# Kernel tuning notes

Hardware: AMD Instinct MI355X
Metric: run time of the kernel (lower is better)

The kernel has to match this reference:

```python
import jax, jax.numpy as jnp
import numpy as np
import math

D = 768; H = 12; DH = 64; LAT = 512; B = 2; L = 1024


def _rms(x, w, eps=1e-6):
    return w * x * jax.lax.rsqrt(jnp.mean(x * x, axis=-1, keepdims=True) + eps)


def _rope_tables(seq_len, dh):
    inv = 1.0 / (10000.0 ** (np.arange(0, dh, 2, dtype=np.float32) / dh))
    t = np.arange(seq_len, dtype=np.float32)
    f = np.outer(t, inv)
    emb = np.concatenate([f, f], axis=-1)
    return jnp.asarray(np.cos(emb))[None, :, None, :], jnp.asarray(np.sin(emb))[None, :, None, :]


def _rope(x, cos, sin):
    x1, x2 = jnp.split(x, 2, axis=-1)
    return x * cos + jnp.concatenate([-x2, x1], axis=-1) * sin


def setup_inputs():
    key = jax.random.key(0)
    ks = jax.random.split(key, 8)
    s = 0.02
    return {
        'x': jax.random.normal(ks[0], (B, L, D), jnp.float32),
        'w_ln': jnp.ones((D,), jnp.float32),
        'w_compress': jax.random.normal(ks[1], (D, LAT), jnp.float32) * s,
        'w_qkv': jax.random.normal(ks[2], (LAT, 3 * D), jnp.float32) * s,
        'w_reso': jax.random.normal(ks[3], (LAT, H * 4), jnp.float32) * s,
        'w_qn': jnp.ones((DH,), jnp.float32),
        'w_kn': jnp.ones((DH,), jnp.float32),
        'head_decay': jnp.linspace(-3.0, 1.0, H).astype(jnp.float32),
        'temperature': jnp.ones((1,), jnp.float32) * 0.5,
        'w_out_gate': jax.random.normal(ks[4], (LAT, D), jnp.float32) * s,
        'w_proj': jax.random.normal(ks[5], (D, D), jnp.float32) * s,
        'w_memnorm': jnp.ones((D,), jnp.float32),
    }


def reference(x, w_ln, w_compress, w_qkv, w_reso, w_qn, w_kn, head_decay, temperature, w_out_gate, w_proj, w_memnorm):
    cos, sin = _rope_tables(L, DH)
    xn = _rms(x, w_ln)
    latent = jax.nn.silu(xn @ w_compress)                        # (B,L,LAT)
    q, k, v = jnp.split(latent @ w_qkv, 3, axis=-1)
    q = _rope(_rms(q.reshape(B, L, H, DH), w_qn), cos, sin)
    k = _rope(_rms(k.reshape(B, L, H, DH), w_kn), cos, sin)
    v_f = v.reshape(B, L, H, DH)
    q_f = jax.nn.elu(q) + 1.0
    k_f = jax.nn.elu(k) + 1.0
    params = (latent @ w_reso).reshape(B, L, H, 4)
    sem_amp, sem_phase, ctx_amp, ctx_phase = [params[..., i] for i in range(4)]
    sem_phase = jax.nn.sigmoid(sem_phase) * math.pi
    ctx_phase = jax.nn.sigmoid(ctx_phase) * math.pi
    decay = jnp.clip(0.3 + 0.65 * jax.nn.sigmoid(head_decay), 1e-5, 0.999)   # (H,)
    gate = jnp.clip(jax.nn.sigmoid(jax.nn.sigmoid(sem_amp) * jax.nn.sigmoid(ctx_amp)
                                   * jnp.cos(sem_phase - ctx_phase) * temperature[0]) * 1.2 - 0.1,
                    0.05, 0.95)                                  # (B,L,H)
    one_m = (1.0 - decay)[None, None, :]                          # (1,1,H)
    kv_in = jnp.einsum('blhd,blhe->blhde', k_f, v_f) * gate[..., None, None] * one_m[..., None, None]
    z_in = k_f * one_m[..., None]
    # cumulative log-decay -> df, same as torch cumsum of constant per-step log_decay
    cum_log = jnp.arange(1, L + 1, dtype=jnp.float32)[:, None] * jnp.log(decay)[None, :]
    df = jnp.exp(cum_log)[None, :, :, None]                       # (1,L,H,1)
    kv_states = jnp.cumsum(kv_in / (df[..., None] + 1e-8), axis=1) * df[..., None]
    z_states = jnp.cumsum(z_in / (df + 1e-8), axis=1) * df
    out_num = jnp.einsum('blhd,blhde->blhe', q_f, kv_states)
    den = jnp.clip(jnp.sum(q_f * z_states, axis=-1, keepdims=True), 1e-5, None)
    out = (out_num / den).reshape(B, L, D)
    return (_rms(out, w_memnorm) @ w_proj) * jax.nn.silu(latent @ w_out_gate)
```

## Files before the change

kernel.cpp:

```cpp
#include <hip/hip_runtime.h>
#include <hip/hip_bf16.h>
#include <math.h>

#define D_MODEL 768
#define NHEAD   12
#define LATD    512
#define BATCH   2
#define SEQ     1024
#define NROWS   (BATCH*SEQ)
#define NCHUNK  (SEQ/64)
#define NBH     (BATCH*NHEAD)
#define NFUSE   3200
#define PQ      72

using short8 = __attribute__((ext_vector_type(8))) short;
using f32x4  = __attribute__((ext_vector_type(4))) float;

__device__ __forceinline__ float sigf(float x){ return 1.f/(1.f+expf(-x)); }
__device__ __forceinline__ float decay_of(float hd){
  float d = 0.3f + 0.65f*sigf(hd);
  return fminf(fmaxf(d, 1e-5f), 0.999f);
}
__device__ __forceinline__ unsigned short f2b(float f){
  __hip_bfloat16 h = __float2bfloat16(f);
  return *reinterpret_cast<unsigned short*>(&h);
}
__device__ __forceinline__ float bf2f(unsigned short u){
  unsigned int x = ((unsigned int)u) << 16;
  return __uint_as_float(x);
}
__device__ __forceinline__ void async16(const unsigned short* g, unsigned short* l){
  __builtin_amdgcn_global_load_lds((const __attribute__((address_space(1))) void*)g,
                                   (__attribute__((address_space(3))) void*)l, 16, 0, 0);
}

__device__ __forceinline__ void rms_row(const float* __restrict__ xr,
    const float* __restrict__ w, unsigned short* __restrict__ yr,
    int tid, float* red)
{
  float v0 = xr[tid], v1 = xr[tid+256], v2 = xr[tid+512];
  float s = v0*v0 + v1*v1 + v2*v2;
  #pragma unroll
  for (int off=32; off; off>>=1) s += __shfl_xor(s, off, 64);
  if ((tid & 63) == 0) red[tid>>6] = s;
  __syncthreads();
  s = red[0]+red[1]+red[2]+red[3];
  float sc = rsqrtf(s*(1.f/(float)D_MODEL) + 1e-6f);
  yr[tid]     = f2b(v0*sc*w[tid]);
  yr[tid+256] = f2b(v1*sc*w[tid+256]);
  yr[tid+512] = f2b(v2*sc*w[tid+512]);
}

__global__ __launch_bounds__(256) void k_rmsnorm_bf(const float* __restrict__ x,
    const float* __restrict__ w, unsigned short* __restrict__ y)
{
  __shared__ float red[4];
  int row = blockIdx.x, tid = threadIdx.x;
  rms_row(x + (size_t)row*D_MODEL, w, y + (size_t)row*D_MODEL, tid, red);
}

__global__ __launch_bounds__(256) void k_prep(
    const float* __restrict__ x, const float* __restrict__ w_ln,
    unsigned short* __restrict__ xn,
    const float* __restrict__ wc, const float* __restrict__ wq,
    const float* __restrict__ wr, const float* __restrict__ wg,
    const float* __restrict__ wp,
    unsigned short* __restrict__ wtc, unsigned short* __restrict__ wtq,
    unsigned short* __restrict__ wtg, unsigned short* __restrict__ wtp)
{
  __shared__ unsigned short tile[64][65];
  __shared__ float red[4];
  int blk = blockIdx.x, t = threadIdx.x;
  if (blk >= 640){
    int row = blk - 640;
    rms_row(x + (size_t)row*D_MODEL, w_ln, xn + (size_t)row*D_MODEL, t, red);
    return;
  }
  const float* W; unsigned short* WT; int K, N, bx, by;
  if (blk < 96){ W=wc; WT=wtc; K=768; N=512; bx=blk&7; by=blk>>3; }
  else if (blk < 384){ int i=blk-96;  W=wq; WT=wtq; K=512; N=2304; bx=i%36; by=i/36; }
  else if (blk < 480){ int i=blk-384; W=wg; WT=wtg; K=512; N=768;  bx=i%12; by=i/12; }
  else if (blk < 624){ int i=blk-480; W=wp; WT=wtp; K=768; N=768;  bx=i%12; by=i/12; }
  else {
    int i = blk - 624;
    #pragma unroll
    for (int j=0;j<16;j++){
      int e = i*4096 + t + j*256;
      int n = 2304 + (e >> 9), k = e & 511;
      float v = (n < 2352) ? wr[(size_t)k*48 + (n-2304)] : 0.f;
      wtq[(size_t)n*512 + k] = f2b(v);
    }
    return;
  }
  int k0 = by*64, n0 = bx*64, cr = t >> 6, cc = t & 63;
  #pragma unroll
  for (int i=0;i<16;i++){
    int r = cr + i*4;
    tile[r][cc] = f2b(W[(size_t)(k0+r)*N + n0 + cc]);
  }
  __syncthreads();
  #pragma unroll
  for (int i=0;i<16;i++){
    int nn = cr + i*4;
    WT[(size_t)(n0+nn)*K + k0 + cc] = tile[cc][nn];
  }
}

__global__ __launch_bounds__(256) void k_gemm64(const unsigned short* __restrict__ A,
    const unsigned short* __restrict__ BT, float* __restrict__ Cf,
    unsigned short* __restrict__ Cb, const unsigned short* __restrict__ auxb,
    int M, int N, int K, int act)
{
  __shared__ unsigned short As[64*64];
  __shared__ unsigned short Bs[64*64];
  int tid = threadIdx.x;
  int w = tid >> 6, lane = tid & 63;
  int m16 = lane & 15, quad = lane >> 4;
  int bm = blockIdx.y*64, bn = blockIdx.x*64;

  f32x4 acc[4];
  #pragma unroll
  for (int nt=0;nt<4;nt++) acc[nt] = (f32x4){0.f,0.f,0.f,0.f};

  for (int kk = 0; kk < K; kk += 64){
    #pragma unroll
    for (int i=0;i<2;i++){
      int g = (w*2 + i)*64 + lane;
      int m = g >> 3, c = (g & 7) ^ (m & 7);
      async16(A  + (size_t)(bm+m)*K + kk + c*8, As + (w*2+i)*512);
      async16(BT + (size_t)(bn+m)*K + kk + c*8, Bs + (w*2+i)*512);
    }
    __syncthreads();
    #pragma unroll
    for (int s=0;s<2;s++){
      int row = w*16 + m16;
      short8 af = *(const short8*)(As + (row*8 + ((s*4 + quad) ^ (row & 7)))*8);
      #pragma unroll
      for (int nt=0;nt<4;nt++){
        int n = nt*16 + m16;
        short8 bf = *(const short8*)(Bs + (n*8 + ((s*4 + quad) ^ (n & 7)))*8);
        acc[nt] = __builtin_amdgcn_mfma_f32_16x16x32_bf16(af, bf, acc[nt], 0, 0, 0);
      }
    }
    __syncthreads();
  }
  #pragma unroll
  for (int r=0;r<4;r++){
    int row = bm + w*16 + quad*4 + r;
    #pragma unroll
    for (int nt=0;nt<4;nt++){
      int col = bn + nt*16 + m16;
      float v = acc[nt][r];
      if (act == 1) v = v/(1.f + __expf(-v));
      else if (act == 2) v *= bf2f(auxb[(size_t)row*N + col]);
      if (Cf) Cf[(size_t)row*N + col] = v;
      if (Cb) Cb[(size_t)row*N + col] = f2b(v);
    }
  }
}

__global__ __launch_bounds__(256) void k_gemm_fused(const unsigned short* __restrict__ A,
    const unsigned short* __restrict__ BT, const float* __restrict__ w_qn,
    const float* __restrict__ w_kn, const float* __restrict__ hdec,
    const float* __restrict__ temp, unsigned short* __restrict__ qf,
    unsigned short* __restrict__ kf, unsigned short* __restrict__ vf,
    float* __restrict__ cKV, float* __restrict__ cG,
    unsigned short* __restrict__ gateb)
{
  __shared__ __align__(16) unsigned short SM[2*128*64];
  unsigned short* As = SM;
  unsigned short* Bs = SM + 128*64;
  const int K = LATD;
  int tid = threadIdx.x;
  int w = tid >> 6, lane = tid & 63;
  int wm = (w >> 1)*64, wn = (w & 1)*64;
  int m16 = lane & 15, quad = lane >> 4;
  int bm = blockIdx.y*128, bn = blockIdx.x*128;

  f32x4 acc[4][4];
  #pragma unroll
  for (int i=0;i<4;i++)
    #pragma unroll
    for (int j=0;j<4;j++) acc[i][j] = (f32x4){0.f,0.f,0.f,0.f};

  for (int kk = 0; kk < K; kk += 64){
    #pragma unroll
    for (int i=0;i<4;i++){
      int g = (w*4 + i)*64 + lane;
      int m = g >> 3, c = (g & 7) ^ (m & 7);
      async16(A  + (size_t)(bm+m)*K + kk + c*8, As + (w*4+i)*512);
      async16(BT + (size_t)(bn+m)*K + kk + c*8, Bs + (w*4+i)*512);
    }
    __syncthreads();
    #pragma unroll
    for (int s=0;s<2;s++){
      short8 af[4], bf[4];
      #pragma unroll
      for (int mt=0;mt<4;mt++){
        int m = wm + mt*16 + m16;
        int idx = m*8 + ((s*4 + quad) ^ (m & 7));
        af[mt] = *(const short8*)(As + idx*8);
      }
      #pragma unroll
      for (int nt=0;nt<4;nt++){
        int n = wn + nt*16 + m16;
        int idx = n*8 + ((s*4 + quad) ^ (n & 7));
        bf[nt] = *(const short8*)(Bs + idx*8);
      }
      #pragma unroll
      for (int mt=0;mt<4;mt++)
        #pragma unroll
        for (int nt=0;nt<4;nt++)
          acc[mt][nt] = __builtin_amdgcn_mfma_f32_16x16x32_bf16(af[mt], bf[nt], acc[mt][nt], 0, 0, 0);
    }
    __syncthreads();
  }

  int colbase = bn + wn;
  if (colbase < 2304){
    int sec = colbase >= 1536 ? 2 : (colbase >= 768 ? 1 : 0);
    int h = (colbase - sec*768) >> 6;
    if (sec == 2){
      #pragma unroll
      for (int mt=0;mt<4;mt++)
        #pragma unroll
        for (int r=0;r<4;r++){
          int row = bm + wm + mt*16 + quad*4 + r;
          int b = row >> 10, t = row & 1023;
          size_t ob = (((size_t)(b*NHEAD+h))*SEQ + t)*64;
          #pragma unroll
          for (int nt=0;nt<4;nt++)
            vf[ob + nt*16 + m16] = f2b(acc[mt][nt][r]);
        }
    } else {
      const float* wnp = sec ? w_kn : w_qn;
      unsigned short* of = sec ? kf : qf;
      float wv4[4];
      #pragma unroll
      for (int nt=0;nt<4;nt++) wv4[nt] = wnp[nt*16 + m16];
      float inv0 = exp2f(-(float)m16*(1.f/32.f)*13.28771237954945f);
      float inv1 = inv0 * 0.01f;
      #pragma unroll
      for (int mt=0;mt<4;mt++)
        #pragma unroll
        for (int r=0;r<4;r++){
          int row = bm + wm + mt*16 + quad*4 + r;
          int b = row >> 10, t = row & 1023;
          float s = 0.f;
          #pragma unroll
          for (int nt=0;nt<4;nt++) s += acc[mt][nt][r]*acc[mt][nt][r];
          s += __shfl_xor(s, 1, 64); s += __shfl_xor(s, 2, 64);
          s += __shfl_xor(s, 4, 64); s += __shfl_xor(s, 8, 64);
          float rs = rsqrtf(s*(1.f/64.f) + 1e-6f);
          float qv[4];
          #pragma unroll
          for (int nt=0;nt<4;nt++) qv[nt] = acc[mt][nt][r]*rs*wv4[nt];
          float s0,c0,s1,c1;
          __sincosf((float)t*inv0, &s0, &c0);
          __sincosf((float)t*inv1, &s1, &c1);
          size_t ob = (((size_t)(b*NHEAD+h))*SEQ + t)*64;
          #pragma unroll
          for (int nt=0;nt<4;nt++){
            float rot = (nt < 2) ? -qv[nt+2] : qv[nt-2];
            float cs = (nt & 1) ? c1 : c0, sn = (nt & 1) ? s1 : s0;
            float val = qv[nt]*cs + rot*sn;
            val = (val > 0.f) ? val + 1.f : __expf(val);
            of[ob + nt*16 + m16] = f2b(val);
          }
        }
    }
  } else if (colbase < 2432){
    float* pf = (float*)SM;
    if (colbase == 2304){
      #pragma unroll
      for (int mt=0;mt<4;mt++)
        #pragma unroll
        for (int r=0;r<4;r++){
          int rowl = wm + mt*16 + quad*4 + r;
          #pragma unroll
          for (int nt=0;nt<4;nt++){
            int p = nt*16 + m16;
            if (p < 48) pf[rowl*49 + p] = acc[mt][nt][r];
          }
        }
    }
    __syncthreads();
    float tv = temp[0];
    #pragma unroll
    for (int i=0;i<6;i++){
      int idx2 = tid + i*256;
      int rowl = idx2 / 12, h = idx2 - rowl*12;
      int row = bm + rowl, b = row >> 10, t = row & 1023;
      const float* pr = pf + rowl*49 + h*4;
      float sa = sigf(pr[0]);
      float sp = sigf(pr[1])*3.14159265358979323846f;
      float ca = sigf(pr[2]);
      float cp = sigf(pr[3])*3.14159265358979323846f;
      float z = sa*ca*cosf(sp - cp)*tv;
      float gate = fminf(fmaxf(sigf(z)*1.2f - 0.1f, 0.05f), 0.95f);
      float dd = decay_of(hdec[h]);
      float df = expf((float)(t+1)*logf(dd));
      float g = df/(df + 1e-8f);
      int ci = (b*NHEAD + h)*SEQ + t;
      cKV[ci] = g*gate*(1.f - dd);
      cG[ci]  = 1.f/gate;
    }
  } else {
    #pragma unroll
    for (int mt=0;mt<4;mt++)
      #pragma unroll
      for (int r=0;r<4;r++){
        int row = bm + wm + mt*16 + quad*4 + r;
        #pragma unroll
        for (int nt=0;nt<4;nt++){
          int gc = colbase + nt*16 + m16 - 2432;
          float v = acc[mt][nt][r];
          v = v/(1.f + __expf(-v));
          gateb[(size_t)row*D_MODEL + gc] = f2b(v);
        }
      }
  }
}

__global__ __launch_bounds__(256) void k_intra(const unsigned short* __restrict__ qf,
    const unsigned short* __restrict__ kf, const unsigned short* __restrict__ vf,
    const float* __restrict__ cKVb, const float* __restrict__ cGb,
    const float* __restrict__ hdec, float* __restrict__ numb,
    float* __restrict__ denb, float* __restrict__ Pb, float* __restrict__ zPb)
{
  __shared__ __align__(16) unsigned short Qb[64*PQ];
  __shared__ __align__(16) unsigned short Kb[64*PQ];
  __shared__ __align__(16) unsigned short KtS[64*PQ];
  __shared__ __align__(16) unsigned short Wb[64*PQ];
  __shared__ __align__(16) unsigned short Vt[80*PQ];
  __shared__ float cn[64], cps[64];
  int bid = blockIdx.x;
  int chunk = bid & 15, bh = bid >> 4, h = bh % NHEAD;
  int tid = threadIdx.x, w = tid >> 6, lane = tid & 63;
  int m16 = lane & 15, quad = lane >> 4;
  size_t base = ((size_t)bh*SEQ + chunk*64)*64;
  float d = decay_of(hdec[h]);
  float l2d = log2f(d);

  if (tid < 64){
    float c = cKVb[bh*SEQ + chunk*64 + tid];
    float pw = exp2f((float)(63 - tid)*l2d);
    cn[tid] = c;
    cps[tid] = c*pw;
    Vt[64*PQ + tid] = f2b(cGb[bh*SEQ + chunk*64 + tid]);
  }
  for (int i = tid; i < 15*PQ; i += 256) Vt[65*PQ + i] = 0;
  __syncthreads();

  #pragma unroll
  for (int i=0;i<2;i++){
    int g = tid + i*256;
    int r = g >> 3, c8 = (g & 7)*8;
    *(short8*)(Qb + r*PQ + c8) = *(const short8*)(qf + base + r*64 + c8);
    *(short8*)(Kb + r*PQ + c8) = *(const short8*)(kf + base + r*64 + c8);
  }
  {
    int s = tid & 63;
    float cpss = cps[s];
    #pragma unroll
    for (int i=0;i<2;i++){
      int c8 = ((tid >> 6) + i*4)*8;
      short8 vv = *(const short8*)(vf + base + s*64 + c8);
      short8 kk = *(const short8*)(kf + base + s*64 + c8);
      #pragma unroll
      for (int j=0;j<8;j++){
        Vt[(c8+j)*PQ + s] = ((unsigned short*)&vv)[j];
        KtS[(c8+j)*PQ + s] = f2b(bf2f(((unsigned short*)&kk)[j])*cpss);
      }
    }
  }
  __syncthreads();

  int trow = w*16 + quad*4;
  for (int stile=0; stile<4; stile++){
    if (stile > w){
      #pragma unroll
      for (int r=0;r<4;r++) Wb[(trow+r)*PQ + stile*16 + m16] = 0;
      continue;
    }
    f32x4 acc = (f32x4){0.f,0.f,0.f,0.f};
    #pragma unroll
    for (int ks=0;ks<2;ks++){
      short8 a = *(const short8*)(Qb + (w*16 + m16)*PQ + ks*32 + quad*8);
      short8 b = *(const short8*)(Kb + (stile*16 + m16)*PQ + ks*32 + quad*8);
      acc = __builtin_amdgcn_mfma_f32_16x16x32_bf16(a, b, acc, 0, 0, 0);
    }
    int s = stile*16 + m16;
    float cns = cn[s];
    #pragma unroll
    for (int r=0;r<4;r++){
      int t = trow + r;
      float wv = 0.f;
      if (s <= t) wv = acc[r]*exp2f((float)(t-s)*l2d)*cns;
      Wb[t*PQ + s] = f2b(wv);
    }
  }
  __syncthreads();

  {
    f32x4 acc[5];
    #pragma unroll
    for (int et=0;et<5;et++) acc[et] = (f32x4){0.f,0.f,0.f,0.f};
    #pragma unroll
    for (int et=0;et<5;et++)
      #pragma unroll
      for (int ks=0;ks<2;ks++){
        short8 a = *(const short8*)(Wb + (w*16 + m16)*PQ + ks*32 + quad*8);
        short8 b = *(const short8*)(Vt + (et*16 + m16)*PQ + ks*32 + quad*8);
        acc[et] = __builtin_amdgcn_mfma_f32_16x16x32_bf16(a, b, acc[et], 0, 0, 0);
      }
    #pragma unroll
    for (int et=0;et<4;et++)
      #pragma unroll
      for (int r=0;r<4;r++)
        numb[base + (size_t)(trow+r)*64 + et*16 + m16] = acc[et][r];
    if (m16 == 0){
      #pragma unroll
      for (int r=0;r<4;r++)
        denb[bh*SEQ + chunk*64 + trow + r] = acc[4][r];
    }
  }
  {
    #pragma unroll
    for (int j=0;j<5;j++){
      int tIdx = w + 4*j;
      int et = tIdx >> 2, dt = tIdx & 3;
      f32x4 acc = (f32x4){0.f,0.f,0.f,0.f};
      #pragma unroll
      for (int ks=0;ks<2;ks++){
        short8 a = *(const short8*)(Vt  + (et*16 + m16)*PQ + ks*32 + quad*8);
        short8 b = *(const short8*)(KtS + (dt*16 + m16)*PQ + ks*32 + quad*8);
        acc = __builtin_amdgcn_mfma_f32_16x16x32_bf16(a, b, acc, 0, 0, 0);
      }
      if (et < 4){
        #pragma unroll
        for (int r=0;r<4;r++)
          Pb[(size_t)bid*4096 + (et*16 + quad*4 + r)*64 + dt*16 + m16] = acc[r];
      } else {
        if (quad == 0) zPb[bid*64 + dt*16 + m16] = acc[0];
      }
    }
  }
}

__global__ __launch_bounds__(256) void k_scan(const float* __restrict__ Pb,
    const float* __restrict__ zPb, unsigned short* __restrict__ Sprev,
    unsigned short* __restrict__ zprev, const float* __restrict__ hdec)
{
  int bh = blockIdx.x >> 2, part = blockIdx.x & 3;
  int h = bh % NHEAD, tid = threadIdx.x;
  float d = decay_of(hdec[h]);
  float d64 = exp2f(64.f*log2f(d));
  int idx = part*1024 + tid*4;
  float4 S = make_float4(0.f,0.f,0.f,0.f);
  for (int c=0;c<NCHUNK;c++){
    size_t off = ((size_t)bh*NCHUNK + c)*4096 + idx;
    unsigned int lo = (unsigned int)f2b(S.x) | ((unsigned int)f2b(S.y) << 16);
    unsigned int hi = (unsigned int)f2b(S.z) | ((unsigned int)f2b(S.w) << 16);
    *(uint2*)(Sprev + off) = make_uint2(lo, hi);
    float4 p = *(const float4*)(Pb + off);
    S.x = S.x*d64 + p.x; S.y = S.y*d64 + p.y;
    S.z = S.z*d64 + p.z; S.w = S.w*d64 + p.w;
  }
  if (part == 0 && tid < 64){
    float z = 0.f;
    for (int c=0;c<NCHUNK;c++){
      int zoff = (bh*NCHUNK + c)*64 + tid;
      zprev[zoff] = f2b(z);
      z = z*d64 + zPb[zoff];
    }
  }
}

__global__ __launch_bounds__(256) void k_cross(const unsigned short* __restrict__ qf,
    const unsigned short* __restrict__ Sprev, const unsigned short* __restrict__ zprev,
    const float* __restrict__ numb, const float* __restrict__ denb,
    const float* __restrict__ hdec, float* __restrict__ attn)
{
  __shared__ __align__(16) unsigned short Qb[64*PQ];
  __shared__ __align__(16) unsigned short Sp[80*PQ];
  __shared__ float den_sm[64];
  int bid = blockIdx.x;
  int chunk = bid & 15, bh = bid >> 4, h = bh % NHEAD, b = bh / NHEAD;
  int tid = threadIdx.x, w = tid >> 6, lane = tid & 63;
  int m16 = lane & 15, quad = lane >> 4;
  size_t base = ((size_t)bh*SEQ + chunk*64)*64;
  float d = decay_of(hdec[h]);
  float l2d = log2f(d);

  #pragma unroll
  for (int i=0;i<2;i++){
    int g = tid + i*256;
    int r = g >> 3, c8 = (g & 7)*8;
    *(short8*)(Qb + r*PQ + c8) = *(const short8*)(qf + base + r*64 + c8);
    *(short8*)(Sp + r*PQ + c8) = *(const short8*)(Sprev + (size_t)bid*4096 + r*64 + c8);
  }
  if (tid < 64) Sp[64*PQ + tid] = zprev[bid*64 + tid];
  for (int i = tid; i < 15*PQ; i += 256) Sp[65*PQ + i] = 0;
  __syncthreads();

  f32x4 acc[5];
  #pragma unroll
  for (int et=0;et<5;et++) acc[et] = (f32x4){0.f,0.f,0.f,0.f};
  #pragma unroll
  for (int et=0;et<5;et++)
    #pragma unroll
    for (int ks=0;ks<2;ks++){
      short8 a = *(const short8*)(Qb + (w*16 + m16)*PQ + ks*32 + quad*8);
      short8 b = *(const short8*)(Sp + (et*16 + m16)*PQ + ks*32 + quad*8);
      acc[et] = __builtin_amdgcn_mfma_f32_16x16x32_bf16(a, b, acc[et], 0, 0, 0);
    }
  int trow = w*16 + quad*4;
  if (m16 == 0){
    #pragma unroll
    for (int r=0;r<4;r++){
      int tl = trow + r;
      float pw = exp2f((float)(tl+1)*l2d);
      float den = fmaxf(denb[bh*SEQ + chunk*64 + tl] + pw*acc[4][r], 1e-5f);
      den_sm[tl] = 1.f/den;
    }
  }
  __syncthreads();
  #pragma unroll
  for (int r=0;r<4;r++){
    int tl = trow + r;
    float pw = exp2f((float)(tl+1)*l2d);
    float invden = den_sm[tl];
    int tg = chunk*64 + tl;
    #pragma unroll
    for (int et=0;et<4;et++){
      int e = et*16 + m16;
      float nm = numb[base + (size_t)tl*64 + e] + pw*acc[et][r];
      attn[((size_t)(b*SEQ + tg))*D_MODEL + h*64 + e] = nm*invden;
    }
  }
}

extern "C" void kernel_launch(void* const* d_in, const int* in_sizes, int n_in,
                              void* d_out, int out_size, void* d_ws, size_t ws_size,
                              hipStream_t stream)
{
  (void)in_sizes; (void)n_in; (void)out_size; (void)ws_size;
  const float* x       = (const float*)d_in[0];
  const float* w_ln    = (const float*)d_in[1];
  const float* w_comp  = (const float*)d_in[2];
  const float* w_qkv   = (const float*)d_in[3];
  const float* w_reso  = (const float*)d_in[4];
  const float* w_qn    = (const float*)d_in[5];
  const float* w_kn    = (const float*)d_in[6];
  const float* hdec    = (const float*)d_in[7];
  const float* temp    = (const float*)d_in[8];
  const float* w_ogate = (const float*)d_in[9];
  const float* w_proj  = (const float*)d_in[10];
  const float* w_mn    = (const float*)d_in[11];
  float* ws = (float*)d_ws;
  float* out = (float*)d_out;

  const size_t o_cKV    = 0;
  const size_t o_cG     = o_cKV    + (size_t)NBH*SEQ;
  const size_t o_den    = o_cG     + (size_t)NBH*SEQ;
  const size_t o_P      = o_den    + (size_t)NBH*SEQ;
  const size_t o_zP     = o_P      + (size_t)NBH*NCHUNK*4096;
  const size_t o_attn   = o_zP     + (size_t)NBH*NCHUNK*64;
  const size_t o_numb   = o_attn   + (size_t)NROWS*D_MODEL;
  const size_t o_end    = o_numb   + (size_t)NBH*SEQ*64;

  unsigned short* bws = (unsigned short*)(ws + o_end);
  const size_t u_xn     = 0;
  const size_t u_latent = u_xn     + (size_t)NROWS*D_MODEL;
  const size_t u_memn   = u_latent + (size_t)NROWS*LATD;
  const size_t u_q      = u_memn   + (size_t)NROWS*D_MODEL;
  const size_t u_k      = u_q      + (size_t)NBH*SEQ*64;
  const size_t u_v      = u_k      + (size_t)NBH*SEQ*64;
  const size_t u_gate   = u_v      + (size_t)NBH*SEQ*64;
  const size_t u_S      = u_gate   + (size_t)NROWS*D_MODEL;
  const size_t u_zprev  = u_S      + (size_t)NBH*NCHUNK*4096;
  const size_t u_wtc    = u_zprev  + (size_t)NBH*NCHUNK*64;
  const size_t u_wtq    = u_wtc    + (size_t)LATD*D_MODEL;
  const size_t u_wtg    = u_wtq    + (size_t)2432*LATD;
  const size_t u_wtp    = u_wtg    + (size_t)D_MODEL*LATD;

  k_prep<<<2688, 256, 0, stream>>>(x, w_ln, bws + u_xn,
      w_comp, w_qkv, w_reso, w_ogate, w_proj,
      bws + u_wtc, bws + u_wtq, bws + u_wtg, bws + u_wtp);
  k_gemm64<<<dim3(LATD/64, NROWS/64), 256, 0, stream>>>(bws + u_xn, bws + u_wtc,
      nullptr, bws + u_latent, nullptr, NROWS, LATD, D_MODEL, 1);
  k_gemm_fused<<<dim3(NFUSE/128, NROWS/128), 256, 0, stream>>>(bws + u_latent, bws + u_wtq,
      w_qn, w_kn, hdec, temp, bws + u_q, bws + u_k, bws + u_v,
      ws + o_cKV, ws + o_cG, bws + u_gate);
  k_intra<<<NBH*NCHUNK, 256, 0, stream>>>(bws + u_q, bws + u_k, bws + u_v,
      ws + o_cKV, ws + o_cG, hdec, ws + o_numb, ws + o_den, ws + o_P, ws + o_zP);
  k_scan<<<NBH*4, 256, 0, stream>>>(ws + o_P, ws + o_zP, bws + u_S, bws + u_zprev, hdec);
  k_cross<<<NBH*NCHUNK, 256, 0, stream>>>(bws + u_q, bws + u_S, bws + u_zprev,
      ws + o_numb, ws + o_den, hdec, ws + o_attn);
  k_rmsnorm_bf<<<NROWS, 256, 0, stream>>>(ws + o_attn, w_mn, bws + u_memn);
  k_gemm64<<<dim3(D_MODEL/64, NROWS/64), 256, 0, stream>>>(bws + u_memn, bws + u_wtp,
      out, nullptr, bws + u_gate, NROWS, D_MODEL, D_MODEL, 2);
}
```

Measured before the change: 156.5 us.

## Fuse intra, scan, cross, memnorm and output GEMM into one cooperative kernel

Merges five kernels (intra-chunk attention, chunk scan, cross-chunk attention, RMS norm and the gated output projection) into a single cooperative kernel separated by grid-wide syncs. The intra-chunk numerator and denominator now stay in registers instead of round-tripping through global memory, which removes the numb/den buffers and several launch gaps. In exchange it adds four grid.sync barriers. The scan phase uses only 96 of 384 blocks, and the GEMM tile and norm loops are tied to the fixed 384-block grid.

New measurement: 347.0 us. +121.8%, slower.

```diff
diff --git a/kernel.cpp b/kernel.cpp
--- a/kernel.cpp
+++ b/kernel.cpp
@@ -1,6 +1,9 @@
 #include <hip/hip_runtime.h>
 #include <hip/hip_bf16.h>
+#include <hip/hip_cooperative_groups.h>
 #include <math.h>
+
+namespace cg = cooperative_groups;
 
 #define D_MODEL 768
 #define NHEAD   12
@@ -10,6 +13,7 @@
 #define NROWS   (BATCH*SEQ)
 #define NCHUNK  (SEQ/64)
 #define NBH     (BATCH*NHEAD)
+#define NCORE   (NBH*NCHUNK)
 #define NFUSE   3200
 #define PQ      72
 
@@ -49,14 +53,6 @@
   yr[tid]     = f2b(v0*sc*w[tid]);
   yr[tid+256] = f2b(v1*sc*w[tid+256]);
   yr[tid+512] = f2b(v2*sc*w[tid+512]);
-}
-
-__global__ __launch_bounds__(256) void k_rmsnorm_bf(const float* __restrict__ x,
-    const float* __restrict__ w, unsigned short* __restrict__ y)
-{
-  __shared__ float red[4];
-  int row = blockIdx.x, tid = threadIdx.x;
-  rms_row(x + (size_t)row*D_MODEL, w, y + (size_t)row*D_MODEL, tid, red);
 }
 
 __global__ __launch_bounds__(256) void k_prep(
@@ -322,22 +318,28 @@
   }
 }
 
-__global__ __launch_bounds__(256) void k_intra(const unsigned short* __restrict__ qf,
-    const unsigned short* __restrict__ kf, const unsigned short* __restrict__ vf,
-    const float* __restrict__ cKVb, const float* __restrict__ cGb,
-    const float* __restrict__ hdec, float* __restrict__ numb,
-    float* __restrict__ denb, float* __restrict__ Pb, float* __restrict__ zPb)
+__global__ __launch_bounds__(256) void k_core(
+    const unsigned short* __restrict__ qf, const unsigned short* __restrict__ kf,
+    const unsigned short* __restrict__ vf, const float* __restrict__ cKVb,
+    const float* __restrict__ cGb, const float* __restrict__ hdec,
+    float* __restrict__ Pb, float* __restrict__ zPb,
+    unsigned short* __restrict__ Sprev, unsigned short* __restrict__ zprev,
+    float* __restrict__ attn, const float* __restrict__ w_mn,
+    unsigned short* __restrict__ memn, const unsigned short* __restrict__ wtp,
+    const unsigned short* __restrict__ gateb, float* __restrict__ out)
 {
+  cg::grid_group grid = cg::this_grid();
   __shared__ __align__(16) unsigned short Qb[64*PQ];
-  __shared__ __align__(16) unsigned short Kb[64*PQ];
-  __shared__ __align__(16) unsigned short KtS[64*PQ];
-  __shared__ __align__(16) unsigned short Wb[64*PQ];
-  __shared__ __align__(16) unsigned short Vt[80*PQ];
-  __shared__ float cn[64], cps[64];
+  __shared__ __align__(16) unsigned short Buf1[80*PQ];
+  __shared__ __align__(16) unsigned short Buf2[64*PQ];
+  __shared__ __align__(16) unsigned short Buf3[64*PQ];
+  __shared__ __align__(16) unsigned short Buf4[64*PQ];
+  __shared__ float cn[64], cps[64], den_sm[64];
   int bid = blockIdx.x;
-  int chunk = bid & 15, bh = bid >> 4, h = bh % NHEAD;
+  int chunk = bid & 15, bh = bid >> 4, h = bh % NHEAD, b = bh / NHEAD;
   int tid = threadIdx.x, w = tid >> 6, lane = tid & 63;
   int m16 = lane & 15, quad = lane >> 4;
+  int trow = w*16 + quad*4;
   size_t base = ((size_t)bh*SEQ + chunk*64)*64;
   float d = decay_of(hdec[h]);
   float l2d = log2f(d);
@@ -347,17 +349,17 @@
     float pw = exp2f((float)(63 - tid)*l2d);
     cn[tid] = c;
     cps[tid] = c*pw;
-    Vt[64*PQ + tid] = f2b(cGb[bh*SEQ + chunk*64 + tid]);
-  }
-  for (int i = tid; i < 15*PQ; i += 256) Vt[65*PQ + i] = 0;
+    Buf1[64*PQ + tid] = f2b(cGb[bh*SEQ + chunk*64 + tid]);
+  }
+  for (int i = tid; i < 15*PQ; i += 256) Buf1[65*PQ + i] = 0;
   __syncthreads();
 
   #pragma unroll
   for (int i=0;i<2;i++){
     int g = tid + i*256;
     int r = g >> 3, c8 = (g & 7)*8;
-    *(short8*)(Qb + r*PQ + c8) = *(const short8*)(qf + base + r*64 + c8);
-    *(short8*)(Kb + r*PQ + c8) = *(const short8*)(kf + base + r*64 + c8);
+    *(short8*)(Qb   + r*PQ + c8) = *(const short8*)(qf + base + r*64 + c8);
+    *(short8*)(Buf2 + r*PQ + c8) = *(const short8*)(kf + base + r*64 + c8);
   }
   {
     int s = tid & 63;
@@ -369,26 +371,25 @@
       short8 kk = *(const short8*)(kf + base + s*64 + c8);
       #pragma unroll
       for (int j=0;j<8;j++){
-        Vt[(c8+j)*PQ + s] = ((unsigned short*)&vv)[j];
-        KtS[(c8+j)*PQ + s] = f2b(bf2f(((unsigned short*)&kk)[j])*cpss);
+        Buf1[(c8+j)*PQ + s] = ((unsigned short*)&vv)[j];
+        Buf3[(c8+j)*PQ + s] = f2b(bf2f(((unsigned short*)&kk)[j])*cpss);
       }
     }
   }
   __syncthreads();
 
-  int trow = w*16 + quad*4;
   for (int stile=0; stile<4; stile++){
     if (stile > w){
       #pragma unroll
-      for (int r=0;r<4;r++) Wb[(trow+r)*PQ + stile*16 + m16] = 0;
+      for (int r=0;r<4;r++) Buf4[(trow+r)*PQ + stile*16 + m16] = 0;
       continue;
     }
     f32x4 acc = (f32x4){0.f,0.f,0.f,0.f};
     #pragma unroll
     for (int ks=0;ks<2;ks++){
-      short8 a = *(const short8*)(Qb + (w*16 + m16)*PQ + ks*32 + quad*8);
-      short8 b = *(const short8*)(Kb + (stile*16 + m16)*PQ + ks*32 + quad*8);
-      acc = __builtin_amdgcn_mfma_f32_16x16x32_bf16(a, b, acc, 0, 0, 0);
+      short8 a = *(const short8*)(Qb   + (w*16 + m16)*PQ + ks*32 + quad*8);
+      short8 bb = *(const short8*)(Buf2 + (stile*16 + m16)*PQ + ks*32 + quad*8);
+      acc = __builtin_amdgcn_mfma_f32_16x16x32_bf16(a, bb, acc, 0, 0, 0);
     }
     int s = stile*16 + m16;
     float cns = cn[s];
@@ -397,34 +398,23 @@
       int t = trow + r;
       float wv = 0.f;
       if (s <= t) wv = acc[r]*exp2f((float)(t-s)*l2d)*cns;
-      Wb[t*PQ + s] = f2b(wv);
+      Buf4[t*PQ + s] = f2b(wv);
     }
   }
   __syncthreads();
 
-  {
-    f32x4 acc[5];
-    #pragma unroll
-    for (int et=0;et<5;et++) acc[et] = (f32x4){0.f,0.f,0.f,0.f};
-    #pragma unroll
-    for (int et=0;et<5;et++)
-      #pragma unroll
-      for (int ks=0;ks<2;ks++){
-        short8 a = *(const short8*)(Wb + (w*16 + m16)*PQ + ks*32 + quad*8);
-        short8 b = *(const short8*)(Vt + (et*16 + m16)*PQ + ks*32 + quad*8);
-        acc[et] = __builtin_amdgcn_mfma_f32_16x16x32_bf16(a, b, acc[et], 0, 0, 0);
-      }
-    #pragma unroll
-    for (int et=0;et<4;et++)
-      #pragma unroll
-      for (int r=0;r<4;r++)
-        numb[base + (size_t)(trow+r)*64 + et*16 + m16] = acc[et][r];
-    if (m16 == 0){
-      #pragma unroll
-      for (int r=0;r<4;r++)
-        denb[bh*SEQ + chunk*64 + trow + r] = acc[4][r];
-    }
-  }
+  f32x4 accN[5];
+  #pragma unroll
+  for (int et=0;et<5;et++) accN[et] = (f32x4){0.f,0.f,0.f,0.f};
+  #pragma unroll
+  for (int et=0;et<5;et++)
+    #pragma unroll
+    for (int ks=0;ks<2;ks++){
+      short8 a = *(const short8*)(Buf4 + (w*16 + m16)*PQ + ks*32 + quad*8);
+      short8 bb = *(const short8*)(Buf1 + (et*16 + m16)*PQ + ks*32 + quad*8);
+      accN[et] = __builtin_amdgcn_mfma_f32_16x16x32_bf16(a, bb, accN[et], 0, 0, 0);
+    }
+
   {
     #pragma unroll
     for (int j=0;j<5;j++){
@@ -433,9 +423,9 @@
       f32x4 acc = (f32x4){0.f,0.f,0.f,0.f};
       #pragma unroll
       for (int ks=0;ks<2;ks++){
-        short8 a = *(const short8*)(Vt  + (et*16 + m16)*PQ + ks*32 + quad*8);
-        short8 b = *(const short8*)(KtS + (dt*16 + m16)*PQ + ks*32 + quad*8);
-        acc = __builtin_amdgcn_mfma_f32_16x16x32_bf16(a, b, acc, 0, 0, 0);
+        short8 a = *(const short8*)(Buf1 + (et*16 + m16)*PQ + ks*32 + quad*8);
+        short8 bb = *(const short8*)(Buf3 + (dt*16 + m16)*PQ + ks*32 + quad*8);
+        acc = __builtin_amdgcn_mfma_f32_16x16x32_bf16(a, bb, acc, 0, 0, 0);
       }
       if (et < 4){
         #pragma unroll
@@ -446,97 +436,139 @@
       }
     }
   }
-}
-
-__global__ __launch_bounds__(256) void k_scan(const float* __restrict__ Pb,
-    const float* __restrict__ zPb, unsigned short* __restrict__ Sprev,
-    unsigned short* __restrict__ zprev, const float* __restrict__ hdec)
-{
-  int bh = blockIdx.x >> 2, part = blockIdx.x & 3;
-  int h = bh % NHEAD, tid = threadIdx.x;
-  float d = decay_of(hdec[h]);
-  float d64 = exp2f(64.f*log2f(d));
-  int idx = part*1024 + tid*4;
-  float4 S = make_float4(0.f,0.f,0.f,0.f);
-  for (int c=0;c<NCHUNK;c++){
-    size_t off = ((size_t)bh*NCHUNK + c)*4096 + idx;
-    unsigned int lo = (unsigned int)f2b(S.x) | ((unsigned int)f2b(S.y) << 16);
-    unsigned int hi = (unsigned int)f2b(S.z) | ((unsigned int)f2b(S.w) << 16);
-    *(uint2*)(Sprev + off) = make_uint2(lo, hi);
-    float4 p = *(const float4*)(Pb + off);
-    S.x = S.x*d64 + p.x; S.y = S.y*d64 + p.y;
-    S.z = S.z*d64 + p.z; S.w = S.w*d64 + p.w;
-  }
-  if (part == 0 && tid < 64){
-    float z = 0.f;
+  grid.sync();
+
+  if (bid < 96){
+    int bh2 = bid >> 2, part = bid & 3;
+    int h2 = bh2 % NHEAD;
+    float d2 = decay_of(hdec[h2]);
+    float d64 = exp2f(64.f*log2f(d2));
+    int idx = part*1024 + tid*4;
+    float4 S = make_float4(0.f,0.f,0.f,0.f);
     for (int c=0;c<NCHUNK;c++){
-      int zoff = (bh*NCHUNK + c)*64 + tid;
-      zprev[zoff] = f2b(z);
-      z = z*d64 + zPb[zoff];
-    }
-  }
-}
-
-__global__ __launch_bounds__(256) void k_cross(const unsigned short* __restrict__ qf,
-    const unsigned short* __restrict__ Sprev, const unsigned short* __restrict__ zprev,
-    const float* __restrict__ numb, const float* __restrict__ denb,
-    const float* __restrict__ hdec, float* __restrict__ attn)
-{
-  __shared__ __align__(16) unsigned short Qb[64*PQ];
-  __shared__ __align__(16) unsigned short Sp[80*PQ];
-  __shared__ float den_sm[64];
-  int bid = blockIdx.x;
-  int chunk = bid & 15, bh = bid >> 4, h = bh % NHEAD, b = bh / NHEAD;
-  int tid = threadIdx.x, w = tid >> 6, lane = tid & 63;
-  int m16 = lane & 15, quad = lane >> 4;
-  size_t base = ((size_t)bh*SEQ + chunk*64)*64;
-  float d = decay_of(hdec[h]);
-  float l2d = log2f(d);
+      size_t off = ((size_t)bh2*NCHUNK + c)*4096 + idx;
+      unsigned int lo = (unsigned int)f2b(S.x) | ((unsigned int)f2b(S.y) << 16);
+      unsigned int hi = (unsigned int)f2b(S.z) | ((unsigned int)f2b(S.w) << 16);
+      *(uint2*)(Sprev + off) = make_uint2(lo, hi);
+      float4 p = *(const float4*)(Pb + off);
+      S.x = S.x*d64 + p.x; S.y = S.y*d64 + p.y;
+      S.z = S.z*d64 + p.z; S.w = S.w*d64 + p.w;
+    }
+    if (part == 0 && tid < 64){
+      float z = 0.f;
+      for (int c=0;c<NCHUNK;c++){
+        int zoff = (bh2*NCHUNK + c)*64 + tid;
+        zprev[zoff] = f2b(z);
+        z = z*d64 + zPb[zoff];
+      }
+    }
+  }
+  grid.sync();
 
   #pragma unroll
   for (int i=0;i<2;i++){
     int g = tid + i*256;
     int r = g >> 3, c8 = (g & 7)*8;
-    *(short8*)(Qb + r*PQ + c8) = *(const short8*)(qf + base + r*64 + c8);
-    *(short8*)(Sp + r*PQ + c8) = *(const short8*)(Sprev + (size_t)bid*4096 + r*64 + c8);
-  }
-  if (tid < 64) Sp[64*PQ + tid] = zprev[bid*64 + tid];
-  for (int i = tid; i < 15*PQ; i += 256) Sp[65*PQ + i] = 0;
+    *(short8*)(Buf1 + r*PQ + c8) = *(const short8*)(Sprev + (size_t)bid*4096 + r*64 + c8);
+  }
+  if (tid < 64) Buf1[64*PQ + tid] = zprev[bid*64 + tid];
   __syncthreads();
 
-  f32x4 acc[5];
-  #pragma unroll
-  for (int et=0;et<5;et++) acc[et] = (f32x4){0.f,0.f,0.f,0.f};
-  #pragma unroll
-  for (int et=0;et<5;et++)
-    #pragma unroll
-    for (int ks=0;ks<2;ks++){
-      short8 a = *(const short8*)(Qb + (w*16 + m16)*PQ + ks*32 + quad*8);
-      short8 b = *(const short8*)(Sp + (et*16 + m16)*PQ + ks*32 + quad*8);
-      acc[et] = __builtin_amdgcn_mfma_f32_16x16x32_bf16(a, b, acc[et], 0, 0, 0);
-    }
-  int trow = w*16 + quad*4;
-  if (m16 == 0){
+  {
+    f32x4 acc2[5];
+    #pragma unroll
+    for (int et=0;et<5;et++) acc2[et] = (f32x4){0.f,0.f,0.f,0.f};
+    #pragma unroll
+    for (int et=0;et<5;et++)
+      #pragma unroll
+      for (int ks=0;ks<2;ks++){
+        short8 a = *(const short8*)(Qb   + (w*16 + m16)*PQ + ks*32 + quad*8);
+        short8 bb = *(const short8*)(Buf1 + (et*16 + m16)*PQ + ks*32 + quad*8);
+        acc2[et] = __builtin_amdgcn_mfma_f32_16x16x32_bf16(a, bb, acc2[et], 0, 0, 0);
+      }
+    if (m16 == 0){
+      #pragma unroll
+      for (int r=0;r<4;r++){
+        int tl = trow + r;
+        float pw = exp2f((float)(tl+1)*l2d);
+        float den = fmaxf(accN[4][r] + pw*acc2[4][r], 1e-5f);
+        den_sm[tl] = 1.f/den;
+      }
+    }
+    __syncthreads();
     #pragma unroll
     for (int r=0;r<4;r++){
       int tl = trow + r;
       float pw = exp2f((float)(tl+1)*l2d);
-      float den = fmaxf(denb[bh*SEQ + chunk*64 + tl] + pw*acc[4][r], 1e-5f);
-      den_sm[tl] = 1.f/den;
-    }
-  }
-  __syncthreads();
-  #pragma unroll
-  for (int r=0;r<4;r++){
-    int tl = trow + r;
-    float pw = exp2f((float)(tl+1)*l2d);
-    float invden = den_sm[tl];
-    int tg = chunk*64 + tl;
-    #pragma unroll
-    for (int et=0;et<4;et++){
-      int e = et*16 + m16;
-      float nm = numb[base + (size_t)tl*64 + e] + pw*acc[et][r];
-      attn[((size_t)(b*SEQ + tg))*D_MODEL + h*64 + e] = nm*invden;
+      float invden = den_sm[tl];
+      int tg = chunk*64 + tl;
+      #pragma unroll
+      for (int et=0;et<4;et++){
+        int e = et*16 + m16;
+        float nm = accN[et][r] + pw*acc2[et][r];
+        attn[((size_t)(b*SEQ + tg))*D_MODEL + h*64 + e] = nm*invden;
+      }
+    }
+  }
+  grid.sync();
+
+  for (int row = bid; row < NROWS; row += NCORE){
+    const float* xr = attn + (size_t)row*D_MODEL;
+    float v0 = xr[tid], v1 = xr[tid+256], v2 = xr[tid+512];
+    float s = v0*v0 + v1*v1 + v2*v2;
+    #pragma unroll
+    for (int off=32; off; off>>=1) s += __shfl_xor(s, off, 64);
+    if ((tid & 63) == 0) den_sm[tid>>6] = s;
+    __syncthreads();
+    s = den_sm[0]+den_sm[1]+den_sm[2]+den_sm[3];
+    float sc = rsqrtf(s*(1.f/(float)D_MODEL) + 1e-6f);
+    unsigned short* yr = memn + (size_t)row*D_MODEL;
+    yr[tid]     = f2b(v0*sc*w_mn[tid]);
+    yr[tid+256] = f2b(v1*sc*w_mn[tid+256]);
+    yr[tid+512] = f2b(v2*sc*w_mn[tid+512]);
+    __syncthreads();
+  }
+  grid.sync();
+
+  {
+    int bx = bid % 12, by = bid / 12;
+    int bm = by*64, bn = bx*64;
+    unsigned short* As = Buf2;
+    unsigned short* Bs = Buf3;
+    f32x4 accg[4];
+    #pragma unroll
+    for (int nt=0;nt<4;nt++) accg[nt] = (f32x4){0.f,0.f,0.f,0.f};
+    for (int kk = 0; kk < D_MODEL; kk += 64){
+      #pragma unroll
+      for (int i=0;i<2;i++){
+        int g = (w*2 + i)*64 + lane;
+        int m = g >> 3, c = (g & 7) ^ (m & 7);
+        async16(memn + (size_t)(bm+m)*D_MODEL + kk + c*8, As + (w*2+i)*512);
+        async16(wtp  + (size_t)(bn+m)*D_MODEL + kk + c*8, Bs + (w*2+i)*512);
+      }
+      __syncthreads();
+      #pragma unroll
+      for (int s=0;s<2;s++){
+        int row = w*16 + m16;
+        short8 af = *(const short8*)(As + (row*8 + ((s*4 + quad) ^ (row & 7)))*8);
+        #pragma unroll
+        for (int nt=0;nt<4;nt++){
+          int n = nt*16 + m16;
+          short8 bf = *(const short8*)(Bs + (n*8 + ((s*4 + quad) ^ (n & 7)))*8);
+          accg[nt] = __builtin_amdgcn_mfma_f32_16x16x32_bf16(af, bf, accg[nt], 0, 0, 0);
+        }
+      }
+      __syncthreads();
+    }
+    #pragma unroll
+    for (int r=0;r<4;r++){
+      int row = bm + w*16 + quad*4 + r;
+      #pragma unroll
+      for (int nt=0;nt<4;nt++){
+        int col = bn + nt*16 + m16;
+        out[(size_t)row*D_MODEL + col] =
+            accg[nt][r]*bf2f(gateb[(size_t)row*D_MODEL + col]);
+      }
     }
   }
 }
@@ -563,12 +595,10 @@
 
   const size_t o_cKV    = 0;
   const size_t o_cG     = o_cKV    + (size_t)NBH*SEQ;
-  const size_t o_den    = o_cG     + (size_t)NBH*SEQ;
-  const size_t o_P      = o_den    + (size_t)NBH*SEQ;
+  const size_t o_P      = o_cG     + (size_t)NBH*SEQ;
   const size_t o_zP     = o_P      + (size_t)NBH*NCHUNK*4096;
   const size_t o_attn   = o_zP     + (size_t)NBH*NCHUNK*64;
-  const size_t o_numb   = o_attn   + (size_t)NROWS*D_MODEL;
-  const size_t o_end    = o_numb   + (size_t)NBH*SEQ*64;
+  const size_t o_end    = o_attn   + (size_t)NROWS*D_MODEL;
 
   unsigned short* bws = (unsigned short*)(ws + o_end);
   const size_t u_xn     = 0;
@@ -593,12 +623,29 @@
   k_gemm_fused<<<dim3(NFUSE/128, NROWS/128), 256, 0, stream>>>(bws + u_latent, bws + u_wtq,
       w_qn, w_kn, hdec, temp, bws + u_q, bws + u_k, bws + u_v,
       ws + o_cKV, ws + o_cG, bws + u_gate);
-  k_intra<<<NBH*NCHUNK, 256, 0, stream>>>(bws + u_q, bws + u_k, bws + u_v,
-      ws + o_cKV, ws + o_cG, hdec, ws + o_numb, ws + o_den, ws + o_P, ws + o_zP);
-  k_scan<<<NBH*4, 256, 0, stream>>>(ws + o_P, ws + o_zP, bws + u_S, bws + u_zprev, hdec);
-  k_cross<<<NBH*NCHUNK, 256, 0, stream>>>(bws + u_q, bws + u_S, bws + u_zprev,
-      ws + o_numb, ws + o_den, hdec, ws + o_attn);
-  k_rmsnorm_bf<<<NROWS, 256, 0, stream>>>(ws + o_attn, w_mn, bws + u_memn);
-  k_gemm64<<<dim3(D_MODEL/64, NROWS/64), 256, 0, stream>>>(bws + u_memn, bws + u_wtp,
-      out, nullptr, bws + u_gate, NROWS, D_MODEL, D_MODEL, 2);
-}
+  {
+    const unsigned short* a_qf   = bws + u_q;
+    const unsigned short* a_kf   = bws + u_k;
+    const unsigned short* a_vf   = bws + u_v;
+    const float*          a_cKV  = ws + o_cKV;
+    const float*          a_cG   = ws + o_cG;
+    const float*          a_hdec = hdec;
+    float*                a_Pb   = ws + o_P;
+    float*                a_zP   = ws + o_zP;
+    unsigned short*       a_S    = bws + u_S;
+    unsigned short*       a_zpr  = bws + u_zprev;
+    float*                a_attn = ws + o_attn;
+    const float*          a_wmn  = w_mn;
+    unsigned short*       a_memn = bws + u_memn;
+    const unsigned short* a_wtp  = bws + u_wtp;
+    const unsigned short* a_gate = bws + u_gate;
+    float*                a_out  = out;
+    void* cargs[] = {
+      (void*)&a_qf, (void*)&a_kf, (void*)&a_vf, (void*)&a_cKV, (void*)&a_cG,
+      (void*)&a_hdec, (void*)&a_Pb, (void*)&a_zP, (void*)&a_S, (void*)&a_zpr,
+      (void*)&a_attn, (void*)&a_wmn, (void*)&a_memn, (void*)&a_wtp,
+      (void*)&a_gate, (void*)&a_out
+    };
+    hipLaunchCooperativeKernel((void*)k_core, dim3(NCORE), dim3(256), cargs, 0, stream);
+  }
+}
```
